# Optimization experiments

Hardware: AMD Instinct MI355X
Metric: run time of the kernel (lower is better)

Reference implementation:

```python
import jax, jax.numpy as jnp
import numpy as np

N, K, D = 1000000, 8, 32


def setup_inputs() -> dict:
    key = jax.random.key(0)
    k_x, k_mu, k_phi = jax.random.split(key, 3)
    X = jax.random.normal(k_x, (N, D), dtype=jnp.float32)
    # Gaussian.__init__: mu = (rand(dims) - 0.5) * 2, sigma = eye(dims)
    mus = (jax.random.uniform(k_mu, (K, D), dtype=jnp.float32) - 0.5) * 2.0
    sigmas = jnp.broadcast_to(jnp.eye(D, dtype=jnp.float32), (K, D, D)).copy()
    # GMM.__init__: phi ~ Dirichlet(1/count); approximate with normalized uniforms
    phi_raw = jax.random.uniform(k_phi, (K,), dtype=jnp.float32) + 1e-3
    phis = phi_raw / phi_raw.sum()
    return {"X": X, "mus": mus, "sigmas": sigmas, "phis": phis}


def reference(X, mus, sigmas, phis):
    # X: [N, D], mus: [K, D], sigmas: [K, D, D], phis: [K]
    d = X.shape[1]
    inv_sigma = jnp.linalg.pinv(sigmas)                      # [K, D, D]
    _, logdet = jnp.linalg.slogdet(sigmas)                   # [K]
    log_two_pi_dims = d * jnp.log(jnp.asarray(2.0 * np.pi, dtype=X.dtype))
    log_den = 0.5 * (log_two_pi_dims + logdet)               # [K]
    diff = X[:, None, :] - mus[None, :, :]                   # [N, K, D]
    # batched Mahalanobis quadratic form: -0.5 * diff @ inv_sigma @ diff^T (diag)
    quad = -0.5 * jnp.einsum('nkd,kde,nke->nk', diff, inv_sigma, diff)  # [N, K]
    # original subtracts exp(log_den), then scales by phi per mixture
    aff = phis[None, :] * (quad - jnp.exp(log_den)[None, :])  # [N, K]
    # ExpNormalizer.exp_norm == row-wise softmax
    return jax.nn.softmax(aff, axis=1)
```

## Files before the change

kernel.cpp:

```cpp
#include <hip/hip_runtime.h>
#include <hip/hip_bf16.h>
#include <math.h>

#define DDIM 32
#define KMIX 8
#define TPW 5

typedef short bf16x8 __attribute__((ext_vector_type(8)));
typedef float f32x4 __attribute__((ext_vector_type(4)));

__global__ __launch_bounds__(1024) void gmm_prep(
    const float* __restrict__ S, const float* __restrict__ mus,
    const float* __restrict__ phis, ushort* __restrict__ Wtg,
    float* __restrict__ amu, float* __restrict__ pa2, float* __restrict__ pc)
{
    __shared__ float aug[DDIM][2 * DDIM + 2];
    __shared__ float pivsave[DDIM];
    __shared__ float amuL[DDIM];
    __shared__ float logL[DDIM];
    const int k = blockIdx.x;
    const int t = threadIdx.x;
    const int r = t >> 5, c = t & 31;

    aug[r][c]      = S[k * 1024 + r * 32 + c];
    aug[r][c + 32] = (c == r) ? 1.f : 0.f;
    __syncthreads();

    for (int p = 0; p < DDIM; ++p) {
        const float piv   = aug[p][p];
        const float f     = aug[r][p];
        const float prow  = aug[p][c];
        const float prow2 = aug[p][c + 32];
        __syncthreads();
        const float ip = 1.f / piv;
        if (r == p) {
            aug[r][c]      = prow * ip;
            aug[r][c + 32] = prow2 * ip;
            if (c == 0) pivsave[p] = piv;
        } else {
            const float fi = f * ip;
            aug[r][c]      = fmaf(-fi, prow,  aug[r][c]);
            aug[r][c + 32] = fmaf(-fi, prow2, aug[r][c + 32]);
        }
        __syncthreads();
    }

    if (t < DDIM) {
        float acc = 0.f;
        for (int d = 0; d < DDIM; ++d)
            acc = fmaf(aug[t][32 + d], mus[k * 32 + d], acc);
        amuL[t] = acc;
        amu[k * 32 + t] = acc;
        logL[t] = logf(fabsf(pivsave[t]));
    }
    __syncthreads();

    {
        const int e = t >> 5, d = t & 31;
        float fv = aug[d][32 + e];
        unsigned u = __builtin_bit_cast(unsigned, fv);
        u = (u + 0x7FFFu + ((u >> 16) & 1u)) >> 16;
        Wtg[k * 1024 + e * 32 + d] = (ushort)u;
    }
    if (t == 0) {
        float ldet = 0.f, muAmu = 0.f;
        for (int i = 0; i < DDIM; ++i) {
            ldet += logL[i];
            muAmu = fmaf(amuL[i], mus[k * 32 + i], muAmu);
        }
        const float eld = expf(0.5f * (DDIM * 1.8378770664093453f + ldet));
        const float LOG2E = 1.4426950408889634f;
        pa2[k] = -0.5f * phis[k] * LOG2E;
        pc[k]  = (-0.5f * phis[k] * muAmu - phis[k] * eld) * LOG2E;
    }
}

template <int CTRL>
__device__ __forceinline__ float dpp_add(float v) {
    int t = __builtin_amdgcn_update_dpp(0, __builtin_bit_cast(int, v), CTRL, 0xF, 0xF, true);
    return v + __builtin_bit_cast(float, t);
}
__device__ __forceinline__ float sel4(float a0, float a1, float a2, float a3, int r) {
    float b0 = (r & 1) ? a1 : a0;
    float b1 = (r & 1) ? a3 : a2;
    return (r & 2) ? b1 : b0;
}

__global__ __launch_bounds__(256, 3) void gmm_main(
    const float* __restrict__ X, const ushort* __restrict__ Wtg,
    const float* __restrict__ amug, const float* __restrict__ pa2g,
    const float* __restrict__ pcg, float* __restrict__ out, int N)
{
    __shared__ float x_s[4][16][36];
    const int tid = threadIdx.x;
    const int lane = tid & 63;
    const int wid = tid >> 6;
    const int g = lane >> 4;
    const int c = lane & 15;

    bf16x8 wf0[KMIX], wf1[KMIX];
#pragma unroll
    for (int k = 0; k < KMIX; ++k) {
        wf0[k] = *(const bf16x8*)(Wtg + (size_t)((k * 32 + c) * 32) + g * 8);
        wf1[k] = *(const bf16x8*)(Wtg + (size_t)((k * 32 + 16 + c) * 32) + g * 8);
    }
    float pa2[KMIX], pc[KMIX];
#pragma unroll
    for (int k = 0; k < KMIX; ++k) { pa2[k] = pa2g[k]; pc[k] = pcg[k]; }
    float n2am0[KMIX], n2am1[KMIX];
#pragma unroll
    for (int k = 0; k < KMIX; ++k) {
        n2am0[k] = -2.f * amug[k * 32 + c];
        n2am1[k] = -2.f * amug[k * 32 + 16 + c];
    }

    const int ntiles = N >> 4;
    const int tile0 = (blockIdx.x * 4 + wid) * TPW;
    const float* lp = X + (size_t)tile0 * 512 + c * 32 + g * 8;

    const int orow = ((lane >> 4) << 2) | (lane & 3);
    const int osel = (lane >> 2) & 3;
    const int rsel = lane & 3;
    const f32x4 zro = {0.f, 0.f, 0.f, 0.f};

    float4 a0 = {0,0,0,0}, a1 = {0,0,0,0};
    if (tile0 < ntiles) { a0 = *(const float4*)lp; a1 = *(const float4*)(lp + 4); }

#pragma unroll
    for (int it = 0; it < TPW; ++it) {
        const int tile = tile0 + it;
        float4 b0 = a0, b1 = a1;
        if (it + 1 < TPW && tile + 1 < ntiles) {
            b0 = *(const float4*)(lp + 512);
            b1 = *(const float4*)(lp + 516);
        }
        if (tile < ntiles) {
            *(float4*)&x_s[wid][c][g * 8]     = a0;
            *(float4*)&x_s[wid][c][g * 8 + 4] = a1;
            int4 xi;
            xi.x = __builtin_amdgcn_perm(__builtin_bit_cast(unsigned, a0.y), __builtin_bit_cast(unsigned, a0.x), 0x07060302u);
            xi.y = __builtin_amdgcn_perm(__builtin_bit_cast(unsigned, a0.w), __builtin_bit_cast(unsigned, a0.z), 0x07060302u);
            xi.z = __builtin_amdgcn_perm(__builtin_bit_cast(unsigned, a1.y), __builtin_bit_cast(unsigned, a1.x), 0x07060302u);
            xi.w = __builtin_amdgcn_perm(__builtin_bit_cast(unsigned, a1.w), __builtin_bit_cast(unsigned, a1.z), 0x07060302u);
            const bf16x8 xf = __builtin_bit_cast(bf16x8, xi);

            float xr0[4], xr1[4];
#pragma unroll
            for (int r = 0; r < 4; ++r) {
                xr0[r] = x_s[wid][g * 4 + r][c];
                xr1[r] = x_s[wid][g * 4 + r][c + 16];
            }
            float ak[KMIX];
#pragma unroll
            for (int k = 0; k < KMIX; ++k) {
                f32x4 acc0 = __builtin_amdgcn_mfma_f32_16x16x32_bf16(xf, wf0[k], zro, 0, 0, 0);
                f32x4 acc1 = __builtin_amdgcn_mfma_f32_16x16x32_bf16(xf, wf1[k], zro, 0, 0, 0);
                float r0 = (acc0[0] + n2am0[k]) * xr0[0] + (acc1[0] + n2am1[k]) * xr1[0];
                float r1 = (acc0[1] + n2am0[k]) * xr0[1] + (acc1[1] + n2am1[k]) * xr1[1];
                float r2 = (acc0[2] + n2am0[k]) * xr0[2] + (acc1[2] + n2am1[k]) * xr1[2];
                float r3 = (acc0[3] + n2am0[k]) * xr0[3] + (acc1[3] + n2am1[k]) * xr1[3];
                r0 = dpp_add<0xB1>(r0); r0 = dpp_add<0x4E>(r0);
                r1 = dpp_add<0xB1>(r1); r1 = dpp_add<0x4E>(r1);
                r2 = dpp_add<0xB1>(r2); r2 = dpp_add<0x4E>(r2);
                r3 = dpp_add<0xB1>(r3); r3 = dpp_add<0x4E>(r3);
                float v = sel4(r0, r1, r2, r3, rsel);
                v = dpp_add<0x124>(v);
                v = dpp_add<0x128>(v);
                ak[k] = fmaf(pa2[k], v, pc[k]);
            }
            float m = ak[0];
#pragma unroll
            for (int k = 1; k < KMIX; ++k) m = fmaxf(m, ak[k]);
            float e[KMIX], s = 0.f;
#pragma unroll
            for (int k = 0; k < KMIX; ++k) { e[k] = __builtin_amdgcn_exp2f(ak[k] - m); s += e[k]; }
            const float inv = 1.f / s;
            float2 o;
            o.x = sel4(e[0], e[2], e[4], e[6], osel) * inv;
            o.y = sel4(e[1], e[3], e[5], e[7], osel) * inv;
            *(float2*)(out + (size_t)(tile * 16 + orow) * 8 + osel * 2) = o;
        }
        a0 = b0; a1 = b1;
        lp += 512;
    }
}

extern "C" void kernel_launch(void* const* d_in, const int* in_sizes, int n_in,
                              void* d_out, int out_size, void* d_ws, size_t ws_size,
                              hipStream_t stream) {
    const float* X    = (const float*)d_in[0];
    const float* mus  = (const float*)d_in[1];
    const float* sig  = (const float*)d_in[2];
    const float* phis = (const float*)d_in[3];
    float* out = (float*)d_out;

    float* ws   = (float*)d_ws;
    float* pa2  = ws;
    float* pc   = ws + 8;
    float* amu  = ws + 16;
    ushort* Wtg = (ushort*)(ws + 272);

    const int N = in_sizes[0] / DDIM;

    gmm_prep<<<KMIX, 1024, 0, stream>>>(sig, mus, phis, Wtg, amu, pa2, pc);

    const int ntiles = N >> 4;
    const int grid = (ntiles + 4 * TPW - 1) / (4 * TPW);
    gmm_main<<<grid, 256, 0, stream>>>(X, Wtg, amu, pa2, pc, out, N);
}
```

Measured before the change: 59.84 us.

## Use Cholesky factor of inverse covariance and MFMA linear term in GMM kernel

The prep kernel now computes a Cholesky factor L of each inverse covariance, so the quadratic term becomes ||L^T x||^2. The main kernel squares the MFMA outputs directly instead of reading x back through shared memory. The linear term phi*A*mu·x is computed with one extra MFMA against a bf16 panel and redistributed with ds_bpermute. The softmax is also spread across lanes with DPP max/sum reductions, which cuts per-lane exp work and removes the LDS staging of X. The cost is extra bf16 rounding on the linear term and a Cholesky step that assumes a positive definite covariance.

Result: slower. 62.41 us (+4.3%).

```diff
diff --git a/kernel.cpp b/kernel.cpp
--- a/kernel.cpp
+++ b/kernel.cpp
@@ -9,12 +9,19 @@
 typedef short bf16x8 __attribute__((ext_vector_type(8)));
 typedef float f32x4 __attribute__((ext_vector_type(4)));
 
+__device__ __forceinline__ ushort to_bf16_rne(float f) {
+    unsigned u = __builtin_bit_cast(unsigned, f);
+    u = (u + 0x7FFFu + ((u >> 16) & 1u)) >> 16;
+    return (ushort)u;
+}
+
 __global__ __launch_bounds__(1024) void gmm_prep(
     const float* __restrict__ S, const float* __restrict__ mus,
     const float* __restrict__ phis, ushort* __restrict__ Wtg,
-    float* __restrict__ amu, float* __restrict__ pa2, float* __restrict__ pc)
+    ushort* __restrict__ Upan, float* __restrict__ pa2, float* __restrict__ pc)
 {
     __shared__ float aug[DDIM][2 * DDIM + 2];
+    __shared__ float ch[DDIM][DDIM + 1];
     __shared__ float pivsave[DDIM];
     __shared__ float amuL[DDIM];
     __shared__ float logL[DDIM];
@@ -50,18 +57,32 @@
         for (int d = 0; d < DDIM; ++d)
             acc = fmaf(aug[t][32 + d], mus[k * 32 + d], acc);
         amuL[t] = acc;
-        amu[k * 32 + t] = acc;
         logL[t] = logf(fabsf(pivsave[t]));
     }
+    ch[r][c] = aug[r][32 + c];
     __syncthreads();
+
+    for (int j = 0; j < DDIM; ++j) {
+        const float djj = ch[j][j];
+        const float cr  = ch[r][j];
+        const float cc  = ch[c][j];
+        __syncthreads();
+        if (c == j) {
+            ch[r][j] = (r >= j) ? cr * rsqrtf(djj) : 0.f;
+        } else if (r > j && c > j) {
+            ch[r][c] = fmaf(-cr * __builtin_amdgcn_rcpf(djj), cc, ch[r][c]);
+        }
+        __syncthreads();
+    }
 
     {
         const int e = t >> 5, d = t & 31;
-        float fv = aug[d][32 + e];
-        unsigned u = __builtin_bit_cast(unsigned, fv);
-        u = (u + 0x7FFFu + ((u >> 16) & 1u)) >> 16;
-        Wtg[k * 1024 + e * 32 + d] = (ushort)u;
-    }
+        const float fv = (d >= e) ? ch[d][e] : 0.f;
+        Wtg[k * 1024 + e * 32 + d] = to_bf16_rne(fv);
+    }
+    if (t < DDIM)
+        Upan[k * 32 + t] = to_bf16_rne(phis[k] * 1.4426950408889634f * amuL[t]);
+    if (k == 0 && t >= 256 && t < 512) Upan[t] = 0;
     if (t == 0) {
         float ldet = 0.f, muAmu = 0.f;
         for (int i = 0; i < DDIM; ++i) {
@@ -80,23 +101,33 @@
     int t = __builtin_amdgcn_update_dpp(0, __builtin_bit_cast(int, v), CTRL, 0xF, 0xF, true);
     return v + __builtin_bit_cast(float, t);
 }
+template <int CTRL>
+__device__ __forceinline__ float dpp_max(float v) {
+    int t = __builtin_amdgcn_update_dpp(0, __builtin_bit_cast(int, v), CTRL, 0xF, 0xF, true);
+    return fmaxf(v, __builtin_bit_cast(float, t));
+}
 __device__ __forceinline__ float sel4(float a0, float a1, float a2, float a3, int r) {
     float b0 = (r & 1) ? a1 : a0;
     float b1 = (r & 1) ? a3 : a2;
     return (r & 2) ? b1 : b0;
 }
+__device__ __forceinline__ float bperm_f(int addr, float v) {
+    return __builtin_bit_cast(float, __builtin_amdgcn_ds_bpermute(addr, __builtin_bit_cast(int, v)));
+}
 
 __global__ __launch_bounds__(256, 3) void gmm_main(
     const float* __restrict__ X, const ushort* __restrict__ Wtg,
-    const float* __restrict__ amug, const float* __restrict__ pa2g,
+    const ushort* __restrict__ Upan, const float* __restrict__ pa2g,
     const float* __restrict__ pcg, float* __restrict__ out, int N)
 {
-    __shared__ float x_s[4][16][36];
     const int tid = threadIdx.x;
     const int lane = tid & 63;
     const int wid = tid >> 6;
     const int g = lane >> 4;
     const int c = lane & 15;
+    const int rsel = c & 3;
+    const int r1 = g * 4 + rsel;
+    const int p = c >> 2;
 
     bf16x8 wf0[KMIX], wf1[KMIX];
 #pragma unroll
@@ -104,25 +135,17 @@
         wf0[k] = *(const bf16x8*)(Wtg + (size_t)((k * 32 + c) * 32) + g * 8);
         wf1[k] = *(const bf16x8*)(Wtg + (size_t)((k * 32 + 16 + c) * 32) + g * 8);
     }
-    float pa2[KMIX], pc[KMIX];
-#pragma unroll
-    for (int k = 0; k < KMIX; ++k) { pa2[k] = pa2g[k]; pc[k] = pcg[k]; }
-    float n2am0[KMIX], n2am1[KMIX];
-#pragma unroll
-    for (int k = 0; k < KMIX; ++k) {
-        n2am0[k] = -2.f * amug[k * 32 + c];
-        n2am1[k] = -2.f * amug[k * 32 + 16 + c];
-    }
+    const bf16x8 uf = *(const bf16x8*)(Upan + c * 32 + g * 8);
+    const float paA = pa2g[2 * p], paB = pa2g[2 * p + 1];
+    const float pcA = pcg[2 * p],  pcB = pcg[2 * p + 1];
+    const int src_byte = (((p >> 1) * 16 + r1) << 2);
 
     const int ntiles = N >> 4;
     const int tile0 = (blockIdx.x * 4 + wid) * TPW;
     const float* lp = X + (size_t)tile0 * 512 + c * 32 + g * 8;
-
-    const int orow = ((lane >> 4) << 2) | (lane & 3);
-    const int osel = (lane >> 2) & 3;
-    const int rsel = lane & 3;
+    float* op = out + (size_t)(tile0 * 16 + r1) * 8 + p * 2;
+
     const f32x4 zro = {0.f, 0.f, 0.f, 0.f};
-
     float4 a0 = {0,0,0,0}, a1 = {0,0,0,0};
     if (tile0 < ntiles) { a0 = *(const float4*)lp; a1 = *(const float4*)(lp + 4); }
 
@@ -135,8 +158,6 @@
             b1 = *(const float4*)(lp + 516);
         }
         if (tile < ntiles) {
-            *(float4*)&x_s[wid][c][g * 8]     = a0;
-            *(float4*)&x_s[wid][c][g * 8 + 4] = a1;
             int4 xi;
             xi.x = __builtin_amdgcn_perm(__builtin_bit_cast(unsigned, a0.y), __builtin_bit_cast(unsigned, a0.x), 0x07060302u);
             xi.y = __builtin_amdgcn_perm(__builtin_bit_cast(unsigned, a0.w), __builtin_bit_cast(unsigned, a0.z), 0x07060302u);
@@ -144,44 +165,50 @@
             xi.w = __builtin_amdgcn_perm(__builtin_bit_cast(unsigned, a1.w), __builtin_bit_cast(unsigned, a1.z), 0x07060302u);
             const bf16x8 xf = __builtin_bit_cast(bf16x8, xi);
 
-            float xr0[4], xr1[4];
-#pragma unroll
-            for (int r = 0; r < 4; ++r) {
-                xr0[r] = x_s[wid][g * 4 + r][c];
-                xr1[r] = x_s[wid][g * 4 + r][c + 16];
-            }
-            float ak[KMIX];
+            const f32x4 lin = __builtin_amdgcn_mfma_f32_16x16x32_bf16(uf, xf, zro, 0, 0, 0);
+
+            float q2[KMIX];
 #pragma unroll
             for (int k = 0; k < KMIX; ++k) {
                 f32x4 acc0 = __builtin_amdgcn_mfma_f32_16x16x32_bf16(xf, wf0[k], zro, 0, 0, 0);
                 f32x4 acc1 = __builtin_amdgcn_mfma_f32_16x16x32_bf16(xf, wf1[k], zro, 0, 0, 0);
-                float r0 = (acc0[0] + n2am0[k]) * xr0[0] + (acc1[0] + n2am1[k]) * xr1[0];
-                float r1 = (acc0[1] + n2am0[k]) * xr0[1] + (acc1[1] + n2am1[k]) * xr1[1];
-                float r2 = (acc0[2] + n2am0[k]) * xr0[2] + (acc1[2] + n2am1[k]) * xr1[2];
-                float r3 = (acc0[3] + n2am0[k]) * xr0[3] + (acc1[3] + n2am1[k]) * xr1[3];
-                r0 = dpp_add<0xB1>(r0); r0 = dpp_add<0x4E>(r0);
-                r1 = dpp_add<0xB1>(r1); r1 = dpp_add<0x4E>(r1);
-                r2 = dpp_add<0xB1>(r2); r2 = dpp_add<0x4E>(r2);
-                r3 = dpp_add<0xB1>(r3); r3 = dpp_add<0x4E>(r3);
-                float v = sel4(r0, r1, r2, r3, rsel);
+                float p0 = fmaf(acc1[0], acc1[0], acc0[0] * acc0[0]);
+                float p1 = fmaf(acc1[1], acc1[1], acc0[1] * acc0[1]);
+                float p2 = fmaf(acc1[2], acc1[2], acc0[2] * acc0[2]);
+                float p3 = fmaf(acc1[3], acc1[3], acc0[3] * acc0[3]);
+                p0 = dpp_add<0xB1>(p0); p0 = dpp_add<0x4E>(p0);
+                p1 = dpp_add<0xB1>(p1); p1 = dpp_add<0x4E>(p1);
+                p2 = dpp_add<0xB1>(p2); p2 = dpp_add<0x4E>(p2);
+                p3 = dpp_add<0xB1>(p3); p3 = dpp_add<0x4E>(p3);
+                float v = sel4(p0, p1, p2, p3, rsel);
                 v = dpp_add<0x124>(v);
                 v = dpp_add<0x128>(v);
-                ak[k] = fmaf(pa2[k], v, pc[k]);
+                q2[k] = v;
             }
-            float m = ak[0];
-#pragma unroll
-            for (int k = 1; k < KMIX; ++k) m = fmaxf(m, ak[k]);
-            float e[KMIX], s = 0.f;
-#pragma unroll
-            for (int k = 0; k < KMIX; ++k) { e[k] = __builtin_amdgcn_exp2f(ak[k] - m); s += e[k]; }
-            const float inv = 1.f / s;
-            float2 o;
-            o.x = sel4(e[0], e[2], e[4], e[6], osel) * inv;
-            o.y = sel4(e[1], e[3], e[5], e[7], osel) * inv;
-            *(float2*)(out + (size_t)(tile * 16 + orow) * 8 + osel * 2) = o;
+
+            const float l0 = bperm_f(src_byte, lin[0]);
+            const float l1 = bperm_f(src_byte, lin[1]);
+            const float l2 = bperm_f(src_byte, lin[2]);
+            const float l3 = bperm_f(src_byte, lin[3]);
+            const float lina = (p & 1) ? l2 : l0;
+            const float linb = (p & 1) ? l3 : l1;
+            const float qa = sel4(q2[0], q2[2], q2[4], q2[6], p);
+            const float qb = sel4(q2[1], q2[3], q2[5], q2[7], p);
+            const float aka = fmaf(paA, qa, pcA) + lina;
+            const float akb = fmaf(paB, qb, pcB) + linb;
+
+            float m = fmaxf(aka, akb);
+            m = dpp_max<0x124>(m); m = dpp_max<0x128>(m);
+            const float ea = __builtin_amdgcn_exp2f(aka - m);
+            const float eb = __builtin_amdgcn_exp2f(akb - m);
+            float s = ea + eb;
+            s = dpp_add<0x124>(s); s = dpp_add<0x128>(s);
+            const float inv = __builtin_amdgcn_rcpf(s);
+            *(float2*)op = make_float2(ea * inv, eb * inv);
         }
         a0 = b0; a1 = b1;
         lp += 512;
+        op += 128;
     }
 }
 
@@ -194,17 +221,17 @@
     const float* phis = (const float*)d_in[3];
     float* out = (float*)d_out;
 
-    float* ws   = (float*)d_ws;
-    float* pa2  = ws;
-    float* pc   = ws + 8;
-    float* amu  = ws + 16;
-    ushort* Wtg = (ushort*)(ws + 272);
+    float* ws    = (float*)d_ws;
+    float* pa2   = ws;
+    float* pc    = ws + 8;
+    ushort* Upan = (ushort*)(ws + 16);
+    ushort* Wtg  = (ushort*)(ws + 272);
 
     const int N = in_sizes[0] / DDIM;
 
-    gmm_prep<<<KMIX, 1024, 0, stream>>>(sig, mus, phis, Wtg, amu, pa2, pc);
+    gmm_prep<<<KMIX, 1024, 0, stream>>>(sig, mus, phis, Wtg, Upan, pa2, pc);
 
     const int ntiles = N >> 4;
     const int grid = (ntiles + 4 * TPW - 1) / (4 * TPW);
-    gmm_main<<<grid, 256, 0, stream>>>(X, Wtg, amu, pa2, pc, out, N);
-}
+    gmm_main<<<grid, 256, 0, stream>>>(X, Wtg, Upan, pa2, pc, out, N);
+}
```
